# Performance work log

Hardware: AMD Instinct MI355X
Metric: run time of the kernel (lower is better)

The kernel has to match this reference:

```python
import jax, jax.numpy as jnp
import numpy as np


def _make_kernels():
    k3 = jnp.array([[0, 1, 0], [1, -4, 1], [0, 1, 0]], dtype=jnp.float32)
    k3 = jnp.tile(k3[None, None], (4, 1, 1, 1))  # [4,1,3,3] depthwise OIHW
    k5 = jnp.array([[0, 0, -1, 0, 0],
                    [0, -1, -2, -1, 0],
                    [-1, -2, 16, -2, -1],
                    [0, -1, -2, -1, 0],
                    [0, 0, -1, 0, 0]], dtype=jnp.float32)
    k5 = jnp.tile(k5[None, None], (4, 1, 1, 1))  # [4,1,5,5]
    return k3, k5


def setup_inputs() -> dict:
    key = jax.random.key(0)
    x = jax.random.normal(key, (32, 4, 512, 512), dtype=jnp.float32)
    k3, k5 = _make_kernels()
    return {"x": x, "k3": k3, "k5": k5}


def _dwconv(x, k, pad):
    # depthwise conv: groups == in_channels == 4
    return jax.lax.conv_general_dilated(
        x, k,
        window_strides=(1, 1),
        padding=((pad, pad), (pad, pad)),
        dimension_numbers=("NCHW", "OIHW", "NCHW"),
        feature_group_count=4,
    )


def reference(x, k3, k5):
    e3 = _dwconv(x, k3, 1)                 # [B,4,H,W]
    e5 = _dwconv(x, k5, 2)                 # [B,4,H,W]
    response = jnp.maximum(jnp.abs(e3), jnp.abs(e5))
    edge_map = jnp.max(response, axis=1, keepdims=True)  # [B,1,H,W]
    v_min = jnp.min(edge_map, axis=(1, 2, 3), keepdims=True)
    v_max = jnp.max(edge_map, axis=(1, 2, 3), keepdims=True)
    return (edge_map - v_min) / (v_max - v_min + 1e-6)
```

## Files before the change

### kernel.cpp

```cpp
#include <hip/hip_runtime.h>

#define IH 512
#define IW 512
#define NC 4
#define NB 32
#define RPT 4

typedef float v4f __attribute__((ext_vector_type(4)));

__global__ void init_minmax(unsigned int* __restrict__ vmin,
                            unsigned int* __restrict__ vmax) {
    int i = threadIdx.x;
    if (i < NB) {
        vmin[i] = 0x7f800000u;
        vmax[i] = 0u;
    }
}

__device__ __forceinline__ void load_row8(const float* __restrict__ xc, int hh,
                                          int w, bool v0, bool v2,
                                          float* __restrict__ dst) {
    if (hh < 0 || hh >= IH) {
        #pragma unroll
        for (int j = 0; j < 8; ++j) dst[j] = 0.f;
        return;
    }
    const float* rowp = xc + (size_t)hh * IW + w;
    float2 a  = v0 ? *(const float2*)(rowp - 2) : float2{0.f, 0.f};
    float4 bb =      *(const float4*)(rowp);
    float2 cc = v2 ? *(const float2*)(rowp + 4) : float2{0.f, 0.f};
    dst[0] = a.x;  dst[1] = a.y;
    dst[2] = bb.x; dst[3] = bb.y; dst[4] = bb.z; dst[5] = bb.w;
    dst[6] = cc.x; dst[7] = cc.y;
}

__global__ __launch_bounds__(256, 4) void edge_kernel(
        const float* __restrict__ x, float* __restrict__ out,
        unsigned int* __restrict__ vmin, unsigned int* __restrict__ vmax) {
    const int qx    = threadIdx.x & 31;
    const int ty    = threadIdx.x >> 5;
    const int w     = blockIdx.x * 128 + qx * 4;
    const int hbase = blockIdx.y * (8 * RPT) + ty * RPT;
    const int b     = blockIdx.z;

    const bool v0 = (w >= 4);
    const bool v2 = (w <= IW - 8);

    float resp[RPT][4];
    #pragma unroll
    for (int k = 0; k < RPT; ++k)
        #pragma unroll
        for (int j = 0; j < 4; ++j) resp[k][j] = 0.f;

    const float* xb = x + (size_t)b * NC * IH * IW;

    #pragma unroll 1
    for (int c = 0; c < NC; ++c) {
        const float* xc = xb + (size_t)c * IH * IW;

        float r[RPT + 4][8];
        #pragma unroll
        for (int rr = 0; rr < RPT + 4; ++rr)
            load_row8(xc, hbase - 2 + rr, w, v0, v2, r[rr]);

        #pragma unroll
        for (int k = 0; k < RPT; ++k) {
            const float* rm2 = r[k + 0];
            const float* rm1 = r[k + 1];
            const float* r0c = r[k + 2];
            const float* rp1 = r[k + 3];
            const float* rp2 = r[k + 4];

            #pragma unroll
            for (int j = 0; j < 4; ++j) {
                const int i = 2 + j;
                const float c0     = r0c[i];
                const float cross1 = rm1[i] + rp1[i] + r0c[i - 1] + r0c[i + 1];
                const float e3     = cross1 - 4.f * c0;
                const float ring   = rm2[i] + rp2[i] + r0c[i - 2] + r0c[i + 2]
                                   + rm1[i - 1] + rm1[i + 1]
                                   + rp1[i - 1] + rp1[i + 1];
                const float e5     = 16.f * c0 - 2.f * cross1 - ring;
                const float rc     = fmaxf(fabsf(e3), fabsf(e5));
                resp[k][j] = fmaxf(resp[k][j], rc);
            }
        }
    }

    float* ob = out + ((size_t)b * IH + hbase) * IW + w;
    #pragma unroll
    for (int k = 0; k < RPT; ++k) {
        float4 o;
        o.x = resp[k][0]; o.y = resp[k][1]; o.z = resp[k][2]; o.w = resp[k][3];
        *(float4*)(ob + (size_t)k * IW) = o;
    }

    float lmin = resp[0][0], lmax = resp[0][0];
    #pragma unroll
    for (int k = 0; k < RPT; ++k)
        #pragma unroll
        for (int j = 0; j < 4; ++j) {
            lmin = fminf(lmin, resp[k][j]);
            lmax = fmaxf(lmax, resp[k][j]);
        }
    #pragma unroll
    for (int off = 32; off >= 1; off >>= 1) {
        lmin = fminf(lmin, __shfl_down(lmin, off));
        lmax = fmaxf(lmax, __shfl_down(lmax, off));
    }
    __shared__ float smin[4], smax[4];
    const int wave = threadIdx.x >> 6;
    const int lane = threadIdx.x & 63;
    if (lane == 0) { smin[wave] = lmin; smax[wave] = lmax; }
    __syncthreads();
    if (threadIdx.x == 0) {
        const float m0 = fminf(fminf(smin[0], smin[1]), fminf(smin[2], smin[3]));
        const float M0 = fmaxf(fmaxf(smax[0], smax[1]), fmaxf(smax[2], smax[3]));
        atomicMin(&vmin[b], __float_as_uint(m0));
        atomicMax(&vmax[b], __float_as_uint(M0));
    }
}

__global__ __launch_bounds__(256) void norm_kernel(
        float* __restrict__ out,
        const unsigned int* __restrict__ vminb,
        const unsigned int* __restrict__ vmaxb) {
    const size_t idx = ((size_t)blockIdx.x * blockDim.x + threadIdx.x) * 8;
    const int b = (int)(idx >> 18);
    const float vmin = __uint_as_float(vminb[b]);
    const float vmax = __uint_as_float(vmaxb[b]);
    const float inv  = 1.0f / (vmax - vmin + 1e-6f);
    v4f u0 = __builtin_nontemporal_load((const v4f*)(out + idx));
    v4f u1 = __builtin_nontemporal_load((const v4f*)(out + idx + 4));
    u0.x = (u0.x - vmin) * inv; u0.y = (u0.y - vmin) * inv;
    u0.z = (u0.z - vmin) * inv; u0.w = (u0.w - vmin) * inv;
    u1.x = (u1.x - vmin) * inv; u1.y = (u1.y - vmin) * inv;
    u1.z = (u1.z - vmin) * inv; u1.w = (u1.w - vmin) * inv;
    __builtin_nontemporal_store(u0, (v4f*)(out + idx));
    __builtin_nontemporal_store(u1, (v4f*)(out + idx + 4));
}

extern "C" void kernel_launch(void* const* d_in, const int* in_sizes, int n_in,
                              void* d_out, int out_size, void* d_ws, size_t ws_size,
                              hipStream_t stream) {
    const float* x = (const float*)d_in[0];
    float* out = (float*)d_out;
    unsigned int* vmin = (unsigned int*)d_ws;
    unsigned int* vmax = vmin + NB;

    hipLaunchKernelGGL(init_minmax, dim3(1), dim3(64), 0, stream, vmin, vmax);
    hipLaunchKernelGGL(edge_kernel, dim3(IW / 128, IH / (8 * RPT), NB), dim3(256),
                       0, stream, x, out, vmin, vmax);
    hipLaunchKernelGGL(norm_kernel, dim3(4096), dim3(256), 0, stream,
                       out, vmin, vmax);
}
```

Before: 220.8 us.

## Fuse edge, min/max reduction and normalization into one cooperative kernel

Replaces the three-kernel pipeline (init, edge, normalize) with a single cooperative kernel. Each block computes two tiles, keeps the responses in registers, and writes per-tile min/max to slots. After a grid-wide sync it reduces its images' slots and stores normalized output directly. This removes the intermediate write and re-read of the output and two launches, at the cost of a grid barrier and doubled register state per thread. If the cooperative launch fails, the old three-kernel path runs instead.

```diff
diff --git a/kernel.cpp b/kernel.cpp
--- a/kernel.cpp
+++ b/kernel.cpp
@@ -1,21 +1,17 @@
 #include <hip/hip_runtime.h>
+#include <hip/hip_cooperative_groups.h>
+
+namespace cg = cooperative_groups;
 
 #define IH 512
 #define IW 512
 #define NC 4
 #define NB 32
 #define RPT 4
+#define NTILES 2048
+#define NBLK 1024
 
 typedef float v4f __attribute__((ext_vector_type(4)));
-
-__global__ void init_minmax(unsigned int* __restrict__ vmin,
-                            unsigned int* __restrict__ vmax) {
-    int i = threadIdx.x;
-    if (i < NB) {
-        vmin[i] = 0x7f800000u;
-        vmax[i] = 0u;
-    }
-}
 
 __device__ __forceinline__ void load_row8(const float* __restrict__ xc, int hh,
                                           int w, bool v0, bool v2,
@@ -34,19 +30,18 @@
     dst[6] = cc.x; dst[7] = cc.y;
 }
 
-__global__ __launch_bounds__(256, 4) void edge_kernel(
-        const float* __restrict__ x, float* __restrict__ out,
-        unsigned int* __restrict__ vmin, unsigned int* __restrict__ vmax) {
-    const int qx    = threadIdx.x & 31;
-    const int ty    = threadIdx.x >> 5;
-    const int w     = blockIdx.x * 128 + qx * 4;
-    const int hbase = blockIdx.y * (8 * RPT) + ty * RPT;
-    const int b     = blockIdx.z;
+__device__ __forceinline__ void compute_tile(const float* __restrict__ x,
+                                             int t, int qx, int tyg,
+                                             float (&resp)[RPT][4]) {
+    const int tx    = t & 3;
+    const int ty    = (t >> 2) & 15;
+    const int b     = t >> 6;
+    const int w     = tx * 128 + qx * 4;
+    const int hbase = ty * (8 * RPT) + tyg * RPT;
 
     const bool v0 = (w >= 4);
     const bool v2 = (w <= IW - 8);
 
-    float resp[RPT][4];
     #pragma unroll
     for (int k = 0; k < RPT; ++k)
         #pragma unroll
@@ -86,6 +81,127 @@
             }
         }
     }
+}
+
+__device__ __forceinline__ void block_minmax_to_slot(
+        const float (&resp)[RPT][4], int t,
+        float* __restrict__ slotmin, float* __restrict__ slotmax,
+        float* __restrict__ smin, float* __restrict__ smax) {
+    float lmin = resp[0][0], lmax = resp[0][0];
+    #pragma unroll
+    for (int k = 0; k < RPT; ++k)
+        #pragma unroll
+        for (int j = 0; j < 4; ++j) {
+            lmin = fminf(lmin, resp[k][j]);
+            lmax = fmaxf(lmax, resp[k][j]);
+        }
+    #pragma unroll
+    for (int off = 32; off >= 1; off >>= 1) {
+        lmin = fminf(lmin, __shfl_down(lmin, off));
+        lmax = fmaxf(lmax, __shfl_down(lmax, off));
+    }
+    const int wave = threadIdx.x >> 6;
+    const int lane = threadIdx.x & 63;
+    if (lane == 0) { smin[wave] = lmin; smax[wave] = lmax; }
+    __syncthreads();
+    if (threadIdx.x == 0) {
+        const float m0 = fminf(fminf(smin[0], smin[1]), fminf(smin[2], smin[3]));
+        const float M0 = fmaxf(fmaxf(smax[0], smax[1]), fmaxf(smax[2], smax[3]));
+        slotmin[t] = m0;
+        slotmax[t] = M0;
+    }
+    __syncthreads();
+}
+
+__device__ __forceinline__ void store_tile(float* __restrict__ out,
+                                           int t, int qx, int tyg,
+                                           const float (&resp)[RPT][4],
+                                           float vmin, float inv) {
+    const int tx    = t & 3;
+    const int ty    = (t >> 2) & 15;
+    const int b     = t >> 6;
+    const int w     = tx * 128 + qx * 4;
+    const int hbase = ty * (8 * RPT) + tyg * RPT;
+
+    float* ob = out + ((size_t)b * IH + hbase) * IW + w;
+    #pragma unroll
+    for (int k = 0; k < RPT; ++k) {
+        v4f o;
+        o.x = (resp[k][0] - vmin) * inv;
+        o.y = (resp[k][1] - vmin) * inv;
+        o.z = (resp[k][2] - vmin) * inv;
+        o.w = (resp[k][3] - vmin) * inv;
+        __builtin_nontemporal_store(o, (v4f*)(ob + (size_t)k * IW));
+    }
+}
+
+__global__ __launch_bounds__(256, 4) void fused_edge(
+        const float* __restrict__ x, float* __restrict__ out,
+        float* __restrict__ slotmin, float* __restrict__ slotmax) {
+    const int qx  = threadIdx.x & 31;
+    const int tyg = threadIdx.x >> 5;
+    const int t0  = blockIdx.x;
+    const int t1  = t0 + NBLK;
+
+    __shared__ float smin[4], smax[4];
+    __shared__ float snorm[4];
+
+    float resp0[RPT][4], resp1[RPT][4];
+    compute_tile(x, t0, qx, tyg, resp0);
+    block_minmax_to_slot(resp0, t0, slotmin, slotmax, smin, smax);
+    compute_tile(x, t1, qx, tyg, resp1);
+    block_minmax_to_slot(resp1, t1, slotmin, slotmax, smin, smax);
+
+    cg::this_grid().sync();
+
+    const int b0 = t0 >> 6;
+    const int wv = threadIdx.x >> 6;
+    const int ln = threadIdx.x & 63;
+    if (wv < 2) {
+        const int img = (wv == 0) ? b0 : (b0 + 16);
+        float mn = slotmin[img * 64 + ln];
+        float mx = slotmax[img * 64 + ln];
+        #pragma unroll
+        for (int off = 32; off >= 1; off >>= 1) {
+            mn = fminf(mn, __shfl_down(mn, off));
+            mx = fmaxf(mx, __shfl_down(mx, off));
+        }
+        if (ln == 0) {
+            snorm[wv * 2]     = mn;
+            snorm[wv * 2 + 1] = 1.0f / (mx - mn + 1e-6f);
+        }
+    }
+    __syncthreads();
+
+    store_tile(out, t0, qx, tyg, resp0, snorm[0], snorm[1]);
+    store_tile(out, t1, qx, tyg, resp1, snorm[2], snorm[3]);
+}
+
+__global__ void init_minmax(unsigned int* __restrict__ vmin,
+                            unsigned int* __restrict__ vmax) {
+    int i = threadIdx.x;
+    if (i < NB) {
+        vmin[i] = 0x7f800000u;
+        vmax[i] = 0u;
+    }
+}
+
+__global__ __launch_bounds__(256, 4) void edge_kernel(
+        const float* __restrict__ x, float* __restrict__ out,
+        unsigned int* __restrict__ vmin, unsigned int* __restrict__ vmax) {
+    const int qx  = threadIdx.x & 31;
+    const int tyg = threadIdx.x >> 5;
+    const int t   = (int)blockIdx.x
+                  + 4 * ((int)blockIdx.y + 16 * (int)blockIdx.z);
+
+    float resp[RPT][4];
+    compute_tile(x, t, qx, tyg, resp);
+
+    const int b     = t >> 6;
+    const int tx    = t & 3;
+    const int ty    = (t >> 2) & 15;
+    const int w     = tx * 128 + qx * 4;
+    const int hbase = ty * (8 * RPT) + tyg * RPT;
 
     float* ob = out + ((size_t)b * IH + hbase) * IW + w;
     #pragma unroll
@@ -145,12 +261,21 @@
                               hipStream_t stream) {
     const float* x = (const float*)d_in[0];
     float* out = (float*)d_out;
-    unsigned int* vmin = (unsigned int*)d_ws;
-    unsigned int* vmax = vmin + NB;
-
-    hipLaunchKernelGGL(init_minmax, dim3(1), dim3(64), 0, stream, vmin, vmax);
-    hipLaunchKernelGGL(edge_kernel, dim3(IW / 128, IH / (8 * RPT), NB), dim3(256),
-                       0, stream, x, out, vmin, vmax);
-    hipLaunchKernelGGL(norm_kernel, dim3(4096), dim3(256), 0, stream,
-                       out, vmin, vmax);
-}
+    float* slotmin = (float*)d_ws;
+    float* slotmax = slotmin + NTILES;
+
+    void* args[] = {(void*)&x, (void*)&out, (void*)&slotmin, (void*)&slotmax};
+    hipError_t err = hipLaunchCooperativeKernel(
+        (const void*)fused_edge, dim3(NBLK), dim3(256), args, 0, stream);
+
+    if (err != hipSuccess) {
+        (void)hipGetLastError();
+        unsigned int* vmin = (unsigned int*)d_ws;
+        unsigned int* vmax = vmin + NB;
+        hipLaunchKernelGGL(init_minmax, dim3(1), dim3(64), 0, stream, vmin, vmax);
+        hipLaunchKernelGGL(edge_kernel, dim3(4, 16, NB), dim3(256), 0, stream,
+                           x, out, vmin, vmax);
+        hipLaunchKernelGGL(norm_kernel, dim3(4096), dim3(256), 0, stream,
+                           out, vmin, vmax);
+    }
+}
```

Result: slower. 338.6 us (+53.4%).
